# Optimization experiments

Measured on AMD Instinct MI355X. Metric: run time of the kernel, lower is better.

## Reference

```python
import jax, jax.numpy as jnp
import numpy as np

# dims: batch, seq, d_model, heads, head_dim, ffn, layers, vocab, group_size
B, S, D, H, DH, DFF, L, V, GS = 2, 1024, 1024, 16, 64, 4096, 2, 32000, 128
EPS = 1e-6


def _dequant(t, s):
    # t: int8 ternary codes [out, in]; s: per-group scales [out*in//GS]
    return (t.reshape(-1, GS).astype(jnp.float32) * s[:, None]).reshape(t.shape)


def _rmsnorm(x, w):
    return x * jax.lax.rsqrt(jnp.mean(x * x, axis=-1, keepdims=True) + EPS) * w


def setup_inputs() -> dict:
    key = jax.random.key(0)
    ks = iter(jax.random.split(key, 64))

    def tern(shape):
        return jax.random.randint(next(ks), shape, -1, 2).astype(jnp.int8)

    def sc(n):
        return jax.random.uniform(next(ks), (n,), minval=0.01, maxval=0.05, dtype=jnp.float32)

    ng_dd = D * D // GS
    ng_fd = DFF * D // GS
    ng_vd = V * D // GS
    inp = {
        'input_ids': jax.random.randint(next(ks), (B, S), 0, V, dtype=jnp.int32),
        'emb_t': tern((V, D)), 'emb_s': sc(ng_vd),
        'qt': tern((L, D, D)), 'qs': jnp.stack([sc(ng_dd) for _ in range(L)]),
        'kt': tern((L, D, D)), 'ks_': jnp.stack([sc(ng_dd) for _ in range(L)]),
        'vt': tern((L, D, D)), 'vs': jnp.stack([sc(ng_dd) for _ in range(L)]),
        'ot': tern((L, D, D)), 'os_': jnp.stack([sc(ng_dd) for _ in range(L)]),
        'gatet': tern((L, DFF, D)), 'gates': jnp.stack([sc(ng_fd) for _ in range(L)]),
        'upt': tern((L, DFF, D)), 'ups': jnp.stack([sc(ng_fd) for _ in range(L)]),
        'downt': tern((L, D, DFF)), 'downs': jnp.stack([sc(ng_fd) for _ in range(L)]),
        'wa': jnp.ones((L, D), jnp.float32),
        'wm': jnp.ones((L, D), jnp.float32),
        'alpha': jnp.full((L, H, 1, 1), 0.5, jnp.float32),
        'wf': jnp.ones((D,), jnp.float32),
        'headt': tern((V, D)), 'heads_': sc(ng_vd),
    }
    return inp


def reference(input_ids, emb_t, emb_s, qt, qs, kt, ks_, vt, vs, ot, os_,
              gatet, gates, upt, ups, downt, downs, wa, wm, alpha, wf,
              headt, heads_):
    # ternary embedding: dequant full table then gather (matches F.embedding on reconstructed weight)
    x = _dequant(emb_t, emb_s)[input_ids]                 # [B, S, D]
    causal = jnp.tril(jnp.ones((S, S), bool))             # [S, S]
    scale = DH ** -0.5
    for l in range(L):
        # --- attention block ---
        h = _rmsnorm(x, wa[l])
        Wq, Wk, Wv, Wo = (_dequant(qt[l], qs[l]), _dequant(kt[l], ks_[l]),
                          _dequant(vt[l], vs[l]), _dequant(ot[l], os_[l]))
        q = (h @ Wq.T).reshape(B, S, H, DH).transpose(0, 2, 1, 3)
        k = (h @ Wk.T).reshape(B, S, H, DH).transpose(0, 2, 1, 3)
        v = (h @ Wv.T).reshape(B, S, H, DH).transpose(0, 2, 1, 3)
        attn = jnp.einsum('bhsd,bhtd->bhst', q, k) * scale
        attn = jnp.where(causal, attn, -jnp.inf)
        p = jax.nn.softmax(attn, axis=-1)
        o = jnp.einsum('bhst,bhtd->bhsd', p, v)
        # per-head residual: alpha * input heads (input to attention is the normed h)
        h_heads = h.reshape(B, S, H, DH).transpose(0, 2, 1, 3)
        o = o + alpha[l] * h_heads
        o = o.transpose(0, 2, 1, 3).reshape(B, S, D)
        x = x + o @ Wo.T
        # --- SwiGLU MLP block ---
        hm = _rmsnorm(x, wm[l])
        Wg, Wu, Wd = (_dequant(gatet[l], gates[l]), _dequant(upt[l], ups[l]),
                      _dequant(downt[l], downs[l]))
        x = x + (jax.nn.silu(hm @ Wg.T) * (hm @ Wu.T)) @ Wd.T
    x = _rmsnorm(x, wf)
    logits = x @ _dequant(headt, heads_).T                # [B, S, V]
    return logits
```

## Files before the change

### kernel.cpp

```cpp
#include <hip/hip_runtime.h>
#include <math.h>
#include <stdint.h>

#define BB   2
#define SS   1024
#define DD   1024
#define HH   16
#define DHH  64
#define DFFD 4096
#define LL   2
#define VV   32000
#define GSZ  128
#define BSR  (BB*SS)
constexpr float EPS = 1e-6f;

typedef unsigned short ushort_t;
typedef __bf16 bf16x8 __attribute__((ext_vector_type(8)));
typedef short  short8 __attribute__((ext_vector_type(8)));
typedef unsigned short ushort8v __attribute__((ext_vector_type(8)));
typedef float  f32x4  __attribute__((ext_vector_type(4)));

__device__ inline ushort_t f2bf(float f) {
    unsigned int u = __builtin_bit_cast(unsigned int, f);
    unsigned int r = u + 0x7fffu + ((u >> 16) & 1u);
    return (ushort_t)(r >> 16);
}
__device__ inline float bf2f(ushort_t u) {
    unsigned int x = ((unsigned int)u) << 16;
    return __builtin_bit_cast(float, x);
}

#define GL2L(g, l) __builtin_amdgcn_global_load_lds( \
    (const __attribute__((address_space(1))) void*)(g), \
    (__attribute__((address_space(3))) void*)(l), 16, 0, 0)

__global__ __launch_bounds__(256) void k_dequant(const int* __restrict__ T,
                                                 const float* __restrict__ S,
                                                 ushort_t* __restrict__ W) {
    int i = (blockIdx.x * 256 + threadIdx.x) * 4;
    int4 t = *(const int4*)(T + i);
    float s = S[i >> 7];
    ushort4 w;
    w.x = f2bf((float)t.x * s); w.y = f2bf((float)t.y * s);
    w.z = f2bf((float)t.z * s); w.w = f2bf((float)t.w * s);
    *(ushort4*)(W + i) = w;
}

__global__ __launch_bounds__(256) void k_dequant_il(const int* __restrict__ T,
                                                    const float* __restrict__ S,
                                                    ushort_t* __restrict__ W,
                                                    int which) {
    int i = (blockIdx.x * 256 + threadIdx.x) * 4;
    int4 t = *(const int4*)(T + i);
    float s = S[i >> 7];
    ushort4 w;
    w.x = f2bf((float)t.x * s); w.y = f2bf((float)t.y * s);
    w.z = f2bf((float)t.z * s); w.w = f2bf((float)t.w * s);
    int r = i >> 10, c = i & 1023;
    *(ushort4*)(W + (((size_t)((r << 1) | which)) << 10) + c) = w;
}

__global__ __launch_bounds__(256) void k_embed(const int* __restrict__ ids,
                                               const int* __restrict__ t,
                                               const float* __restrict__ s,
                                               float* __restrict__ x) {
    int row = blockIdx.x;
    int id  = ids[row];
    for (int d = threadIdx.x; d < DD; d += 256) {
        x[(size_t)row * DD + d] =
            (float)t[(size_t)id * DD + d] * s[id * (DD / GSZ) + (d >> 7)];
    }
}

__global__ __launch_bounds__(256) void k_rmsnorm(const float* __restrict__ x,
                                                 const float* __restrict__ w,
                                                 ushort_t* __restrict__ o) {
    int row = blockIdx.x;
    const float* xr = x + (size_t)row * DD;
    float ss = 0.f;
    for (int d = threadIdx.x; d < DD; d += 256) { float v = xr[d]; ss += v * v; }
    __shared__ float sm[4];
    for (int off = 32; off > 0; off >>= 1) ss += __shfl_down(ss, off, 64);
    if ((threadIdx.x & 63) == 0) sm[threadIdx.x >> 6] = ss;
    __syncthreads();
    float tot = sm[0] + sm[1] + sm[2] + sm[3];
    float inv = rsqrtf(tot / DD + EPS);
    for (int d = threadIdx.x; d < DD; d += 256)
        o[(size_t)row * DD + d] = f2bf(xr[d] * inv * w[d]);
}

template <int MODE>
__global__ __launch_bounds__(256) void gemm_bf16(const ushort_t* __restrict__ A,
                                                 const ushort_t* __restrict__ W,
                                                 float* __restrict__ Cf,
                                                 ushort_t* __restrict__ Cb,
                                                 int M, int N, int K) {
    __shared__ ushort_t As[128 * 32];
    __shared__ ushort_t Bs[128 * 32];
    const int tid  = threadIdx.x;
    const int wave = tid >> 6, lane = tid & 63;
    const int wm = wave >> 1, wn = wave & 1;

    const int nwg  = gridDim.x;
    const int orig = blockIdx.x;
    const int wgid = (orig & 7) * (nwg >> 3) + (orig >> 3);
    const int i0 = (wgid & 15) * 128;
    const int o0 = (wgid >> 4) * 128;

    f32x4 acc[4][4] = {};

    const int srow = wave * 32 + (lane >> 2);
    const int scol = (lane & 3) * 8;
    const ushort_t* aG0 = A + (size_t)(i0 + srow) * K + scol;
    const ushort_t* aG1 = aG0 + (size_t)16 * K;
    const ushort_t* bG0 = W + (size_t)(o0 + srow) * K + scol;
    const ushort_t* bG1 = bG0 + (size_t)16 * K;
    ushort_t* aL0 = As + wave * 1024;
    ushort_t* aL1 = aL0 + 512;
    ushort_t* bL0 = Bs + wave * 1024;
    ushort_t* bL1 = bL0 + 512;

    const ushort_t* ap = As + (wm * 64 + (lane & 15)) * 32 + (lane >> 4) * 8;
    const ushort_t* bp = Bs + (wn * 64 + (lane & 15)) * 32 + (lane >> 4) * 8;

    for (int k0 = 0; k0 < K; k0 += 32) {
        __syncthreads();
        GL2L(aG0 + k0, aL0);
        GL2L(aG1 + k0, aL1);
        GL2L(bG0 + k0, bL0);
        GL2L(bG1 + k0, bL1);
        __syncthreads();
        bf16x8 av[4], bv[4];
#pragma unroll
        for (int t = 0; t < 4; ++t) {
            av[t] = __builtin_bit_cast(bf16x8, *(const short8*)(ap + t * 512));
            bv[t] = __builtin_bit_cast(bf16x8, *(const short8*)(bp + t * 512));
        }
#pragma unroll
        for (int mt = 0; mt < 4; ++mt)
#pragma unroll
            for (int nt = 0; nt < 4; ++nt)
                acc[mt][nt] = __builtin_amdgcn_mfma_f32_16x16x32_bf16(
                    av[mt], bv[nt], acc[mt][nt], 0, 0, 0);
    }

    const int r0 = wm * 64 + (lane >> 4) * 4;
    const int c0 = wn * 64 + (lane & 15);
#pragma unroll
    for (int mt = 0; mt < 4; ++mt) {
#pragma unroll
        for (int r = 0; r < 4; ++r) {
            const size_t row = i0 + r0 + mt * 16 + r;
#pragma unroll
            for (int nt = 0; nt < 4; ++nt) {
                const size_t col = o0 + c0 + nt * 16;
                const size_t idx = row * (size_t)N + col;
                float v = acc[mt][nt][r];
                if (MODE == 0) {
                    Cf[idx] = v;
                } else if (MODE == 1) {
                    Cf[idx] += v;
                } else if (MODE == 3) {
                    Cb[idx] = f2bf(v);
                } else {
                    float pv = __shfl_xor(v, 1, 64);
                    if (!(lane & 1)) {
                        float g = v, u = pv;
                        float res = g / (1.f + __expf(-g)) * u;
                        Cb[row * (size_t)(N >> 1) + (col >> 1)] = f2bf(res);
                    }
                }
            }
        }
    }
}

__global__ __launch_bounds__(256) void k_fattn(const ushort_t* __restrict__ qkv,
                                               const ushort_t* __restrict__ hn,
                                               const float* __restrict__ alpha,
                                               ushort_t* __restrict__ out) {
    __shared__ ushort_t Ks[64][72];
    __shared__ ushort_t Vt[64][72];
    __shared__ ushort_t Ps[4][16][72];

    const int bid = blockIdx.x;
    const int bh  = bid & 31;
    const int qt  = 15 - (bid >> 5);
    const int hh  = bh & 15;
    const int b   = bh >> 4;
    const int tid = threadIdx.x;
    const int wm  = tid >> 6;
    const int ln  = tid & 63;
    const int m16 = ln & 15;
    const int q4  = ln >> 4;

    const int bS0 = b * SS;
    const int q0  = qt * 64 + wm * 16;

    bf16x8 qa0, qa1;
    {
        const ushort_t* qp = qkv + (size_t)(bS0 + q0 + m16) * 3072 + hh * DHH + q4 * 8;
        qa0 = __builtin_bit_cast(bf16x8, *(const ushort8v*)(qp));
        qa1 = __builtin_bit_cast(bf16x8, *(const ushort8v*)(qp + 32));
    }

    f32x4 oacc[4] = {};
    float mrow[4] = {-1e30f, -1e30f, -1e30f, -1e30f};
    float lrow[4] = {0.f, 0.f, 0.f, 0.f};

    const int c0a = tid, c1a = tid + 256;
    const int r0a = c0a >> 3, cc0 = (c0a & 7) * 8;
    const int r1a = c1a >> 3, cc1 = (c1a & 7) * 8;

    for (int t = 0; t <= qt; ++t) {
        __syncthreads();
        {
            const size_t kbase = (size_t)(bS0 + t * 64) * 3072 + 1024 + hh * DHH;
            *(ushort8v*)&Ks[r0a][cc0] = *(const ushort8v*)(qkv + kbase + (size_t)r0a * 3072 + cc0);
            *(ushort8v*)&Ks[r1a][cc1] = *(const ushort8v*)(qkv + kbase + (size_t)r1a * 3072 + cc1);
            const size_t vbase = (size_t)(bS0 + t * 64) * 3072 + 2048 + hh * DHH;
            ushort8v v0 = *(const ushort8v*)(qkv + vbase + (size_t)r0a * 3072 + cc0);
#pragma unroll
            for (int j = 0; j < 8; ++j) Vt[cc0 + j][r0a] = v0[j];
            ushort8v v1 = *(const ushort8v*)(qkv + vbase + (size_t)r1a * 3072 + cc1);
#pragma unroll
            for (int j = 0; j < 8; ++j) Vt[cc1 + j][r1a] = v1[j];
        }
        __syncthreads();

        f32x4 sc[4];
#pragma unroll
        for (int nt = 0; nt < 4; ++nt) {
            bf16x8 kb0 = __builtin_bit_cast(bf16x8, *(const ushort8v*)&Ks[nt * 16 + m16][q4 * 8]);
            bf16x8 kb1 = __builtin_bit_cast(bf16x8, *(const ushort8v*)&Ks[nt * 16 + m16][32 + q4 * 8]);
            f32x4 z = {};
            z = __builtin_amdgcn_mfma_f32_16x16x32_bf16(qa0, kb0, z, 0, 0, 0);
            sc[nt] = __builtin_amdgcn_mfma_f32_16x16x32_bf16(qa1, kb1, z, 0, 0, 0);
        }

        const bool diag = (t == qt);
#pragma unroll
        for (int r = 0; r < 4; ++r) {
            float s0 = sc[0][r] * 0.125f;
            float s1 = sc[1][r] * 0.125f;
            float s2 = sc[2][r] * 0.125f;
            float s3 = sc[3][r] * 0.125f;
            if (diag) {
                const int rl = wm * 16 + q4 * 4 + r;
                if (m16      > rl) s0 = -1e30f;
                if (m16 + 16 > rl) s1 = -1e30f;
                if (m16 + 32 > rl) s2 = -1e30f;
                if (m16 + 48 > rl) s3 = -1e30f;
            }
            float tm = fmaxf(fmaxf(s0, s1), fmaxf(s2, s3));
            tm = fmaxf(tm, __shfl_xor(tm, 1, 64));
            tm = fmaxf(tm, __shfl_xor(tm, 2, 64));
            tm = fmaxf(tm, __shfl_xor(tm, 4, 64));
            tm = fmaxf(tm, __shfl_xor(tm, 8, 64));
            const float mnew = fmaxf(mrow[r], tm);
            const float corr = __expf(mrow[r] - mnew);
            const float e0 = __expf(s0 - mnew);
            const float e1 = __expf(s1 - mnew);
            const float e2 = __expf(s2 - mnew);
            const float e3 = __expf(s3 - mnew);
            float rs = e0 + e1 + e2 + e3;
            rs += __shfl_xor(rs, 1, 64);
            rs += __shfl_xor(rs, 2, 64);
            rs += __shfl_xor(rs, 4, 64);
            rs += __shfl_xor(rs, 8, 64);
            lrow[r] = lrow[r] * corr + rs;
            mrow[r] = mnew;
#pragma unroll
            for (int dt = 0; dt < 4; ++dt) oacc[dt][r] *= corr;
            const int pr = q4 * 4 + r;
            Ps[wm][pr][m16]      = f2bf(e0);
            Ps[wm][pr][m16 + 16] = f2bf(e1);
            Ps[wm][pr][m16 + 32] = f2bf(e2);
            Ps[wm][pr][m16 + 48] = f2bf(e3);
        }

#pragma unroll
        for (int ks = 0; ks < 2; ++ks) {
            bf16x8 pa = __builtin_bit_cast(bf16x8, *(const ushort8v*)&Ps[wm][m16][ks * 32 + q4 * 8]);
#pragma unroll
            for (int dt = 0; dt < 4; ++dt) {
                bf16x8 vb = __builtin_bit_cast(bf16x8, *(const ushort8v*)&Vt[dt * 16 + m16][ks * 32 + q4 * 8]);
                oacc[dt] = __builtin_amdgcn_mfma_f32_16x16x32_bf16(pa, vb, oacc[dt], 0, 0, 0);
            }
        }
    }

    const float al = alpha[hh];
#pragma unroll
    for (int r = 0; r < 4; ++r) {
        const float inv = 1.f / lrow[r];
        const size_t row = (size_t)(bS0 + q0 + q4 * 4 + r);
#pragma unroll
        for (int dt = 0; dt < 4; ++dt) {
            const size_t idx = row * DD + hh * DHH + dt * 16 + m16;
            out[idx] = f2bf(oacc[dt][r] * inv + al * bf2f(hn[idx]));
        }
    }
}

extern "C" void kernel_launch(void* const* d_in, const int* in_sizes, int n_in,
                              void* d_out, int out_size, void* d_ws, size_t ws_size,
                              hipStream_t stream) {
    const int*   ids   = (const int*)d_in[0];
    const int*   emb_t = (const int*)d_in[1];
    const float* emb_s = (const float*)d_in[2];
    const int*   qt    = (const int*)d_in[3];
    const float* qs    = (const float*)d_in[4];
    const int*   kt    = (const int*)d_in[5];
    const float* ks    = (const float*)d_in[6];
    const int*   vt    = (const int*)d_in[7];
    const float* vs    = (const float*)d_in[8];
    const int*   ot    = (const int*)d_in[9];
    const float* os    = (const float*)d_in[10];
    const int*   gatet = (const int*)d_in[11];
    const float* gates = (const float*)d_in[12];
    const int*   upt   = (const int*)d_in[13];
    const float* ups   = (const float*)d_in[14];
    const int*   downt = (const int*)d_in[15];
    const float* downs = (const float*)d_in[16];
    const float* wa    = (const float*)d_in[17];
    const float* wm    = (const float*)d_in[18];
    const float* alpha = (const float*)d_in[19];
    const float* wf    = (const float*)d_in[20];
    const int*   headt = (const int*)d_in[21];
    const float* heads = (const float*)d_in[22];

    const size_t MB = 1ull << 20;
    char* wsb = (char*)d_ws;
    ushort_t* wbuf = (ushort_t*)(wsb);
    ushort_t* gb   = (ushort_t*)(wsb + 58 * MB);
    float*    x    = (float*)   (wsb + 75 * MB);
    ushort_t* h    = (ushort_t*)(wsb + 84 * MB);
    ushort_t* qkvb = (ushort_t*)(wsb + 89 * MB);
    ushort_t* ao   = (ushort_t*)(wsb + 102 * MB);

    const size_t wDD = (size_t)DD * DD;
    const size_t sDD = wDD / GSZ;
    const size_t wFD = (size_t)DFFD * DD;
    const size_t sFD = wFD / GSZ;

    k_embed<<<BSR, 256, 0, stream>>>(ids, emb_t, emb_s, x);

    for (int l = 0; l < LL; ++l) {
        k_rmsnorm<<<BSR, 256, 0, stream>>>(x, wa + l * DD, h);
        k_dequant<<<wDD / 1024, 256, 0, stream>>>(qt + l * wDD, qs + l * sDD, wbuf);
        k_dequant<<<wDD / 1024, 256, 0, stream>>>(kt + l * wDD, ks + l * sDD, wbuf + wDD);
        k_dequant<<<wDD / 1024, 256, 0, stream>>>(vt + l * wDD, vs + l * sDD, wbuf + 2 * wDD);
        gemm_bf16<3><<<24 * 16, 256, 0, stream>>>(h, wbuf, nullptr, qkvb, BSR, 3072, DD);
        k_fattn<<<16 * BB * HH, 256, 0, stream>>>(qkvb, h, alpha + l * HH, ao);
        k_dequant<<<wDD / 1024, 256, 0, stream>>>(ot + l * wDD, os + l * sDD, wbuf);
        gemm_bf16<1><<<8 * 16, 256, 0, stream>>>(ao, wbuf, x, nullptr, BSR, DD, DD);

        k_rmsnorm<<<BSR, 256, 0, stream>>>(x, wm + l * DD, h);
        k_dequant_il<<<wFD / 1024, 256, 0, stream>>>(gatet + l * wFD, gates + l * sFD, wbuf, 0);
        k_dequant_il<<<wFD / 1024, 256, 0, stream>>>(upt + l * wFD, ups + l * sFD, wbuf, 1);
        gemm_bf16<4><<<64 * 16, 256, 0, stream>>>(h, wbuf, nullptr, gb, BSR, 8192, DD);
        k_dequant<<<wFD / 1024, 256, 0, stream>>>(downt + l * wFD, downs + l * sFD, wbuf);
        gemm_bf16<1><<<8 * 16, 256, 0, stream>>>(gb, wbuf, x, nullptr, BSR, DD, DFFD);
    }

    k_rmsnorm<<<BSR, 256, 0, stream>>>(x, wf, h);
    k_dequant<<<((size_t)VV * DD) / 1024, 256, 0, stream>>>(headt, heads, wbuf);
    gemm_bf16<0><<<250 * 16, 256, 0, stream>>>(h, wbuf, (float*)d_out, nullptr, BSR, VV, DD);
}
```

Before: 1.217 ms.

## Add 256x256 double-buffered GEMM kernel for gate/up and LM-head projections

Introduces a new 512-thread GEMM with 256x256 output tiles, swizzled LDS layout, double-buffered global-to-LDS staging interleaved with MFMA phases, and grid remapping for L2 locality. It replaces the smaller-tile GEMM for the fused gate/up SwiGLU projection and the vocabulary head. The aim is higher arithmetic intensity and overlap of loads with matrix math on the two largest GEMMs. It trades this for heavy register and LDS use (128KB shared) and fragile hand-written waitcnt/barrier sequencing. The old GEMM's epilogue is cut down to only the accumulate and bf16 store modes.

```diff
diff --git a/kernel.cpp b/kernel.cpp
--- a/kernel.cpp
+++ b/kernel.cpp
@@ -156,17 +156,142 @@
                 const size_t col = o0 + c0 + nt * 16;
                 const size_t idx = row * (size_t)N + col;
                 float v = acc[mt][nt][r];
+                if (MODE == 1) Cf[idx] += v;
+                else           Cb[idx] = f2bf(v);
+            }
+        }
+    }
+}
+
+#define BAR()    __builtin_amdgcn_s_barrier()
+#define WAITL0() do { asm volatile("s_waitcnt lgkmcnt(0)" ::: "memory"); \
+                      __builtin_amdgcn_sched_barrier(0); } while (0)
+#define WAITV4() asm volatile("s_waitcnt vmcnt(4)" ::: "memory")
+
+#define STG(gbase, sbase, tile, half, call) do {                          \
+    int _ko = (tile) * 64; if (_ko > K - 64) _ko = K - 64;                \
+    GL2L((gbase) + (size_t)((half) * 128 + (call) * 64) * K + _ko,        \
+         (sbase) + (half) * 8192 + (call) * 4096); } while (0)
+
+#define RD_B(so) do { _Pragma("unroll") for (int nf = 0; nf < 4; ++nf) {  \
+    bfr[nf][0] = __builtin_bit_cast(bf16x8, *(const short8*)(rB + (so) + nf * 1024 + colA0)); \
+    bfr[nf][1] = __builtin_bit_cast(bf16x8, *(const short8*)(rB + (so) + nf * 1024 + colA1)); } } while (0)
+
+#define RD_A(so, mf0) do { _Pragma("unroll") for (int i = 0; i < 2; ++i) { \
+    afr[i][0] = __builtin_bit_cast(bf16x8, *(const short8*)(rA + (so) + ((mf0) + i) * 1024 + colA0)); \
+    afr[i][1] = __builtin_bit_cast(bf16x8, *(const short8*)(rA + (so) + ((mf0) + i) * 1024 + colA1)); } } while (0)
+
+#define MFMA16(mf0) do {                                                   \
+    __builtin_amdgcn_s_setprio(1);                                         \
+    _Pragma("unroll") for (int i = 0; i < 2; ++i)                          \
+    _Pragma("unroll") for (int nf = 0; nf < 4; ++nf) {                     \
+        acc[(mf0) + i][nf] = __builtin_amdgcn_mfma_f32_16x16x32_bf16(      \
+            afr[i][0], bfr[nf][0], acc[(mf0) + i][nf], 0, 0, 0);           \
+        acc[(mf0) + i][nf] = __builtin_amdgcn_mfma_f32_16x16x32_bf16(      \
+            afr[i][1], bfr[nf][1], acc[(mf0) + i][nf], 0, 0, 0); }         \
+    __builtin_amdgcn_s_setprio(0); } while (0)
+
+template <int MODE>
+__global__ __launch_bounds__(512, 2) void gemm256(const ushort_t* __restrict__ A,
+                                                  const ushort_t* __restrict__ W,
+                                                  float* __restrict__ Cf,
+                                                  ushort_t* __restrict__ Cb,
+                                                  int N, int K) {
+    __shared__ ushort_t smem[65536];
+
+    const int tid = threadIdx.x;
+    const int w   = tid >> 6;
+    const int l   = tid & 63;
+    const int wm  = w >> 2;
+    const int wn  = w & 3;
+    const int m16 = l & 15;
+    const int q4  = l >> 4;
+
+    const int nwg  = gridDim.x;
+    const int orig = blockIdx.x;
+    const int wgid = (orig & 7) * (nwg >> 3) + (orig >> 3);
+    const int i0   = (wgid & 7) * 256;
+    const int o0   = (wgid >> 3) * 256;
+
+    const int sc = ((l & 7) * 8) ^ ((l & 32) ? 16 : 0) ^ ((w & 1) ? 8 : 0)
+                                 ^ ((l & 8) ? 32 : 0);
+    const int srow = w * 8 + (l >> 3);
+    const ushort_t* gA = A + (size_t)(i0 + srow) * K + sc;
+    const ushort_t* gB = W + (size_t)(o0 + srow) * K + sc;
+    ushort_t* sA0 = smem + w * 512;
+    ushort_t* sA1 = sA0 + 16384;
+    ushort_t* sB0 = sA0 + 32768;
+    ushort_t* sB1 = sA0 + 49152;
+
+    const int colA0 = (q4 * 8) ^ ((l & 1) << 5) ^ ((l & 4) << 2) ^ (l & 8);
+    const int colA1 = colA0 ^ 32;
+    const ushort_t* rA = smem + (wm * 128 + m16) * 64;
+    const ushort_t* rB = smem + 32768 + (wn * 64 + m16) * 64;
+
+    f32x4 acc[8][4] = {};
+    bf16x8 bfr[4][2];
+    bf16x8 afr[2][2];
+
+    STG(gB, sB0, 0, 0, 0); STG(gB, sB0, 0, 0, 1);
+    STG(gB, sB0, 0, 1, 0); STG(gB, sB0, 0, 1, 1);
+    STG(gA, sA0, 0, 0, 0); STG(gA, sA0, 0, 0, 1);
+    STG(gA, sA0, 0, 1, 0); STG(gA, sA0, 0, 1, 1);
+    STG(gB, sB1, 1, 0, 0); STG(gB, sB1, 1, 0, 1);
+    STG(gB, sB1, 1, 1, 0); STG(gB, sB1, 1, 1, 1);
+    WAITV4();
+    BAR();
+
+    const int niter = K >> 7;
+    for (int it = 0; it < niter; ++it) {
+        const int t0 = it * 2;
+        RD_B(0); RD_A(0, 0);
+        STG(gA, sA1, t0 + 1, 0, 0); STG(gA, sA1, t0 + 1, 0, 1);
+        STG(gA, sA1, t0 + 1, 1, 0); STG(gA, sA1, t0 + 1, 1, 1);
+        BAR(); WAITL0(); MFMA16(0); BAR();
+        RD_A(0, 2);
+        STG(gB, sB0, t0 + 2, 0, 0); STG(gB, sB0, t0 + 2, 0, 1);
+        BAR(); WAITL0(); MFMA16(2); BAR();
+        RD_A(0, 4);
+        STG(gB, sB0, t0 + 2, 1, 0); STG(gB, sB0, t0 + 2, 1, 1);
+        BAR(); WAITL0(); MFMA16(4); BAR();
+        RD_A(0, 6);
+        BAR(); WAITL0(); MFMA16(6);
+        WAITV4(); BAR();
+        RD_B(16384); RD_A(16384, 0);
+        STG(gA, sA0, t0 + 2, 0, 0); STG(gA, sA0, t0 + 2, 0, 1);
+        BAR(); WAITL0(); MFMA16(0); BAR();
+        RD_A(16384, 2);
+        STG(gA, sA0, t0 + 2, 1, 0); STG(gA, sA0, t0 + 2, 1, 1);
+        BAR(); WAITL0(); MFMA16(2); BAR();
+        RD_A(16384, 4);
+        STG(gB, sB1, t0 + 3, 0, 0); STG(gB, sB1, t0 + 3, 0, 1);
+        BAR(); WAITL0(); MFMA16(4); BAR();
+        RD_A(16384, 6);
+        STG(gB, sB1, t0 + 3, 1, 0); STG(gB, sB1, t0 + 3, 1, 1);
+        BAR(); WAITL0(); MFMA16(6);
+        WAITV4(); BAR();
+    }
+
+    asm volatile("s_waitcnt vmcnt(0) lgkmcnt(0)" ::: "memory");
+    BAR();
+
+    const int r0 = i0 + wm * 128 + q4 * 4;
+    const int c0 = o0 + wn * 64 + m16;
+#pragma unroll
+    for (int mf = 0; mf < 8; ++mf) {
+#pragma unroll
+        for (int rr = 0; rr < 4; ++rr) {
+            const size_t row = r0 + mf * 16 + rr;
+#pragma unroll
+            for (int nf = 0; nf < 4; ++nf) {
+                const size_t col = c0 + nf * 16;
+                float v = acc[mf][nf][rr];
                 if (MODE == 0) {
-                    Cf[idx] = v;
-                } else if (MODE == 1) {
-                    Cf[idx] += v;
-                } else if (MODE == 3) {
-                    Cb[idx] = f2bf(v);
+                    Cf[row * (size_t)N + col] = v;
                 } else {
                     float pv = __shfl_xor(v, 1, 64);
-                    if (!(lane & 1)) {
-                        float g = v, u = pv;
-                        float res = g / (1.f + __expf(-g)) * u;
+                    if (!(l & 1)) {
+                        float res = v / (1.f + __expf(-v)) * pv;
                         Cb[row * (size_t)(N >> 1) + (col >> 1)] = f2bf(res);
                     }
                 }
@@ -359,12 +484,12 @@
         k_rmsnorm<<<BSR, 256, 0, stream>>>(x, wm + l * DD, h);
         k_dequant_il<<<wFD / 1024, 256, 0, stream>>>(gatet + l * wFD, gates + l * sFD, wbuf, 0);
         k_dequant_il<<<wFD / 1024, 256, 0, stream>>>(upt + l * wFD, ups + l * sFD, wbuf, 1);
-        gemm_bf16<4><<<64 * 16, 256, 0, stream>>>(h, wbuf, nullptr, gb, BSR, 8192, DD);
+        gemm256<4><<<32 * 8, 512, 0, stream>>>(h, wbuf, nullptr, gb, 8192, DD);
         k_dequant<<<wFD / 1024, 256, 0, stream>>>(downt + l * wFD, downs + l * sFD, wbuf);
         gemm_bf16<1><<<8 * 16, 256, 0, stream>>>(gb, wbuf, x, nullptr, BSR, DD, DFFD);
     }
 
     k_rmsnorm<<<BSR, 256, 0, stream>>>(x, wf, h);
     k_dequant<<<((size_t)VV * DD) / 1024, 256, 0, stream>>>(headt, heads, wbuf);
-    gemm_bf16<0><<<250 * 16, 256, 0, stream>>>(h, wbuf, (float*)d_out, nullptr, BSR, VV, DD);
-}
+    gemm256<0><<<125 * 8, 512, 0, stream>>>(h, wbuf, (float*)d_out, nullptr, VV, DD);
+}
```

Measured after the change: 1.185 ms. -2.6%, faster.
